# Optimization experiments

Measured on AMD Instinct MI355X. Metric: run time of the kernel, lower is better.

## Reference

```python
import jax, jax.numpy as jnp
import numpy as np


def gru_step(x, h, W, U, b):
    # Keras GRU, reset_after=True. W:[in,3H] U:[H,3H] b:[2,3H]
    gi = x @ W + b[0]
    gh = h @ U + b[1]
    iz, ir, ih = jnp.split(gi, 3, axis=-1)
    hz, hr, hh = jnp.split(gh, 3, axis=-1)
    z = jax.nn.sigmoid(iz + hz)
    r = jax.nn.sigmoid(ir + hr)
    n = jnp.tanh(ih + r * hh)
    return z * h + (1.0 - z) * n


def gru_seq(x, W, U, b):
    # x: [B,S,in] -> outputs [B,S,H], last state [B,H]; zero initial state
    B = x.shape[0]
    H = U.shape[0]
    h0 = jnp.zeros((B, H), x.dtype)
    def step(h, xt):
        h2 = gru_step(xt, h, W, U, b)
        return h2, h2
    hT, ys = jax.lax.scan(step, h0, jnp.swapaxes(x, 0, 1))
    return jnp.swapaxes(ys, 0, 1), hT


def setup_inputs() -> dict:
    key = jax.random.key(0)
    ks = jax.random.split(key, 24)
    V_en, V_fr, E, H = 32000, 32000, 256, 1024
    B, S = 32, 48
    s = 0.05
    d = {}
    d["inputs"] = jax.random.randint(ks[0], (B, S), 0, V_en, dtype=jnp.int32)
    d["gen_seq_len"] = 32
    d["start_id"] = 1
    d["emb_en"] = jax.random.normal(ks[1], (V_en, E), jnp.float32) * s
    d["emb_fr"] = jax.random.normal(ks[2], (V_fr, E), jnp.float32) * s
    # encoder GRUs: layer0 in=E, layer1 in=H
    d["enc_W0"] = jax.random.normal(ks[3], (E, 3 * H), jnp.float32) * s
    d["enc_U0"] = jax.random.normal(ks[4], (H, 3 * H), jnp.float32) * s
    d["enc_b0"] = jnp.zeros((2, 3 * H), jnp.float32)
    d["enc_W1"] = jax.random.normal(ks[5], (H, 3 * H), jnp.float32) * s
    d["enc_U1"] = jax.random.normal(ks[6], (H, 3 * H), jnp.float32) * s
    d["enc_b1"] = jnp.zeros((2, 3 * H), jnp.float32)
    # decoder GRUs: layer0 in = H(context)+E(embed), layer1 in = H
    d["dec_W0"] = jax.random.normal(ks[7], (H + E, 3 * H), jnp.float32) * s
    d["dec_U0"] = jax.random.normal(ks[8], (H, 3 * H), jnp.float32) * s
    d["dec_b0"] = jnp.zeros((2, 3 * H), jnp.float32)
    d["dec_W1"] = jax.random.normal(ks[9], (H, 3 * H), jnp.float32) * s
    d["dec_U1"] = jax.random.normal(ks[10], (H, 3 * H), jnp.float32) * s
    d["dec_b1"] = jnp.zeros((2, 3 * H), jnp.float32)
    # Bahdanau attention
    d["attn_W1"] = jax.random.normal(ks[11], (H, H), jnp.float32) * s
    d["attn_b1"] = jnp.zeros((H,), jnp.float32)
    d["attn_W2"] = jax.random.normal(ks[12], (H, H), jnp.float32) * s
    d["attn_b2"] = jnp.zeros((H,), jnp.float32)
    d["attn_V"] = jax.random.normal(ks[13], (H, 1), jnp.float32) * s
    d["attn_Vb"] = jnp.zeros((1,), jnp.float32)
    # output projection
    d["fc_W"] = jax.random.normal(ks[14], (H, V_fr), jnp.float32) * s
    d["fc_b"] = jnp.zeros((V_fr,), jnp.float32)
    return d


def reference(inputs, gen_seq_len, start_id, emb_en, emb_fr,
              enc_W0, enc_U0, enc_b0, enc_W1, enc_U1, enc_b1,
              dec_W0, dec_U0, dec_b0, dec_W1, dec_U1, dec_b1,
              attn_W1, attn_b1, attn_W2, attn_b2, attn_V, attn_Vb,
              fc_W, fc_b):
    B = inputs.shape[0]
    H = enc_U0.shape[0]
    V_fr = fc_W.shape[1]
    # ---- encoder ----
    x = emb_en[inputs]                       # [B,S,E]
    x, _ = gru_seq(x, enc_W0, enc_U0, enc_b0)
    enc_out, enc_hidden = gru_seq(x, enc_W1, enc_U1, enc_b1)  # [B,S,H], [B,H]
    # precompute W2(values) (same math as recomputing per step)
    enc_proj = enc_out @ attn_W2 + attn_b2   # [B,S,H]
    zeros_h = jnp.zeros((B, H), jnp.float32)

    def dec_step(carry, _):
        dec_in, hidden = carry
        # Bahdanau attention
        q = hidden @ attn_W1 + attn_b1                          # [B,H]
        score = jnp.tanh(q[:, None, :] + enc_proj) @ attn_V + attn_Vb  # [B,S,1]
        w = jax.nn.softmax(score, axis=1)
        ctx = jnp.sum(w * enc_out, axis=1)                      # [B,H]
        xt = jnp.concatenate([ctx, emb_fr[dec_in]], axis=-1)    # [B,H+E]
        # decoder GRUs with state reset to zero each step (initial_state=None)
        h1 = gru_step(xt, zeros_h, dec_W0, dec_U0, dec_b0)
        h2 = gru_step(h1, zeros_h, dec_W1, dec_U1, dec_b1)
        logits = h2 @ fc_W + fc_b                               # [B,V_fr]
        nxt = jnp.argmax(logits, axis=1).astype(jnp.int32)
        return (nxt, h2), logits

    dec_in0 = jnp.full((B,), start_id, dtype=jnp.int32)
    (_, _), logits_seq = jax.lax.scan(dec_step, (dec_in0, enc_hidden),
                                      None, length=gen_seq_len - 1)
    first = jax.nn.one_hot(dec_in0, V_fr, dtype=jnp.float32)[:, None, :]
    return jnp.concatenate([first, jnp.swapaxes(logits_seq, 0, 1)], axis=1)
```

## Files before the change

kernel.cpp:

```cpp
#include <hip/hip_runtime.h>
#include <math.h>

#define BB 32
#define SS 48
#define HH 1024
#define EE 256
#define VOC 32000
#define GEN 32
#define G3 3072
#define CH 256
#define NLOG (VOC / 128)

typedef float v4f __attribute__((ext_vector_type(4)));

__device__ __forceinline__ float sigf(float x) { return 1.f / (1.f + expf(-x)); }

__global__ __launch_bounds__(256) void embed_en_k(const int* __restrict__ inputs,
                                                  const float* __restrict__ emb,
                                                  float* __restrict__ x) {
    int i = blockIdx.x * 256 + threadIdx.x;
    int row = i >> 8;
    int e = i & 255;
    x[i] = emb[(size_t)inputs[row] * EE + e];
}

__global__ __launch_bounds__(256) void transpose_k(const float* __restrict__ U,
                                                   float* __restrict__ UT,
                                                   int R, int C) {
    __shared__ float t[32][33];
    int tx = threadIdx.x & 31, ty = threadIdx.x >> 5;
    int bx = blockIdx.x * 32;
    int by = blockIdx.y * 32;
#pragma unroll
    for (int i = 0; i < 4; ++i)
        t[ty + 8 * i][tx] = U[(size_t)(by + ty + 8 * i) * C + bx + tx];
    __syncthreads();
#pragma unroll
    for (int i = 0; i < 4; ++i)
        UT[(size_t)(bx + ty + 8 * i) * R + by + tx] = t[tx][ty + 8 * i];
}

__global__ __launch_bounds__(256) void gemm64(const float* __restrict__ A,
                                              const float* __restrict__ Bm,
                                              const float* __restrict__ bias,
                                              float* __restrict__ C,
                                              int N, int K) {
    __shared__ float As[32][68];
    __shared__ float Bs[32][68];
    int tid = threadIdx.x;
    int tx = tid & 15, ty = tid >> 4;
    int arow = blockIdx.y * 64, bcol = blockIdx.x * 64;
    int am = tid >> 2;
    int aq = tid & 3;
    int bk = tid >> 4;
    int bn = tid & 15;
    float acc[4][4] = {};
    for (int k0 = 0; k0 < K; k0 += 32) {
        float4 a0 = *(const float4*)(A + (size_t)(arow + am) * K + k0 + aq * 8);
        float4 a1 = *(const float4*)(A + (size_t)(arow + am) * K + k0 + aq * 8 + 4);
        float4 b0 = *(const float4*)(Bm + (size_t)(k0 + bk) * N + bcol + bn * 4);
        float4 b1 = *(const float4*)(Bm + (size_t)(k0 + bk + 16) * N + bcol + bn * 4);
        __syncthreads();
        As[aq * 8 + 0][am] = a0.x; As[aq * 8 + 1][am] = a0.y;
        As[aq * 8 + 2][am] = a0.z; As[aq * 8 + 3][am] = a0.w;
        As[aq * 8 + 4][am] = a1.x; As[aq * 8 + 5][am] = a1.y;
        As[aq * 8 + 6][am] = a1.z; As[aq * 8 + 7][am] = a1.w;
        *(float4*)&Bs[bk][bn * 4] = b0;
        *(float4*)&Bs[bk + 16][bn * 4] = b1;
        __syncthreads();
#pragma unroll
        for (int kk = 0; kk < 32; ++kk) {
            float4 a = *(const float4*)&As[kk][ty * 4];
            float4 b = *(const float4*)&Bs[kk][tx * 4];
            acc[0][0] += a.x * b.x; acc[0][1] += a.x * b.y;
            acc[0][2] += a.x * b.z; acc[0][3] += a.x * b.w;
            acc[1][0] += a.y * b.x; acc[1][1] += a.y * b.y;
            acc[1][2] += a.y * b.z; acc[1][3] += a.y * b.w;
            acc[2][0] += a.z * b.x; acc[2][1] += a.z * b.y;
            acc[2][2] += a.z * b.z; acc[2][3] += a.z * b.w;
            acc[3][0] += a.w * b.x; acc[3][1] += a.w * b.y;
            acc[3][2] += a.w * b.z; acc[3][3] += a.w * b.w;
        }
    }
    float4 bb = *(const float4*)&bias[bcol + tx * 4];
#pragma unroll
    for (int i = 0; i < 4; ++i) {
        size_t row = arow + ty * 4 + i;
        *(float4*)(C + row * N + bcol + tx * 4) =
            make_float4(acc[i][0] + bb.x, acc[i][1] + bb.y,
                        acc[i][2] + bb.z, acc[i][3] + bb.w);
    }
}

__global__ __launch_bounds__(384) void enc_step(
    const float* __restrict__ gi,
    const float* __restrict__ UT,
    const float* __restrict__ b1,
    const float* __restrict__ hin,
    float* __restrict__ hout,
    float* __restrict__ seqout,
    int t) {
    __shared__ float hs[32][260];
    __shared__ float ghs[12][33];
    const int tid = threadIdx.x;
    const int c0 = blockIdx.x * 4;
    const int ks = tid & 31;
    const int outIdx = tid >> 5;
    const int cq = outIdx >> 2;
    const int mo = outIdx & 3;
    const float* Ubase = UT + (size_t)(cq * HH + c0) * HH;
    float acc[4][8];
#pragma unroll
    for (int a = 0; a < 4; ++a)
#pragma unroll
        for (int b = 0; b < 8; ++b) acc[a][b] = 0.f;
    for (int ch = 0; ch < HH / CH; ++ch) {
        for (int i = tid; i < 32 * 64; i += 384) {
            int m = i >> 6, q = i & 63;
            *(float4*)&hs[m][q * 4] =
                *(const float4*)&hin[m * HH + ch * CH + q * 4];
        }
        __syncthreads();
#pragma unroll
        for (int j = 0; j < 2; ++j) {
            int kq = (j * 32 + ks) * 4;
            float4 uv[4];
#pragma unroll
            for (int ci = 0; ci < 4; ++ci)
                uv[ci] = *(const float4*)&Ubase[(size_t)ci * HH + ch * CH + kq];
#pragma unroll
            for (int mi = 0; mi < 8; ++mi) {
                float4 hv = *(const float4*)&hs[mo * 8 + mi][kq];
#pragma unroll
                for (int ci = 0; ci < 4; ++ci)
                    acc[ci][mi] += hv.x * uv[ci].x + hv.y * uv[ci].y +
                                   hv.z * uv[ci].z + hv.w * uv[ci].w;
            }
        }
        __syncthreads();
    }
#pragma unroll
    for (int ci = 0; ci < 4; ++ci)
#pragma unroll
        for (int mi = 0; mi < 8; ++mi) {
            float v = acc[ci][mi];
            v += __shfl_xor(v, 1, 64);
            v += __shfl_xor(v, 2, 64);
            v += __shfl_xor(v, 4, 64);
            v += __shfl_xor(v, 8, 64);
            v += __shfl_xor(v, 16, 64);
            if (ks == 0) ghs[cq * 4 + ci][mo * 8 + mi] = v;
        }
    __syncthreads();
    if (tid < 128) {
        int m = tid & 31, c = tid >> 5;
        int col = c0 + c;
        float ghz = ghs[c][m] + b1[col];
        float ghr = ghs[4 + c][m] + b1[HH + col];
        float ghh = ghs[8 + c][m] + b1[2 * HH + col];
        const float* gir = gi + ((size_t)m * SS + t) * G3;
        float z = sigf(gir[col] + ghz);
        float r = sigf(gir[HH + col] + ghr);
        float nn = tanhf(gir[2 * HH + col] + r * ghh);
        float h = z * hin[m * HH + col] + (1.f - z) * nn;
        hout[m * HH + col] = h;
        seqout[((size_t)m * SS + t) * HH + col] = h;
    }
}

__global__ __launch_bounds__(384) void dec_step(
    const float* __restrict__ xt, int K,
    const float* __restrict__ WT,
    const float* __restrict__ b0, const float* __restrict__ b1,
    float* __restrict__ hout) {
    __shared__ float hs[32][260];
    __shared__ float ghs[12][33];
    const int tid = threadIdx.x;
    const int c0 = blockIdx.x * 4;
    const int ks = tid & 31;
    const int outIdx = tid >> 5;
    const int cq = outIdx >> 2;
    const int mo = outIdx & 3;
    const float* Ubase = WT + (size_t)(cq * HH + c0) * K;
    float acc[4][8];
#pragma unroll
    for (int a = 0; a < 4; ++a)
#pragma unroll
        for (int b = 0; b < 8; ++b) acc[a][b] = 0.f;
    const int nch = K / CH;
    for (int ch = 0; ch < nch; ++ch) {
        for (int i = tid; i < 32 * 64; i += 384) {
            int m = i >> 6, q = i & 63;
            *(float4*)&hs[m][q * 4] =
                *(const float4*)&xt[(size_t)m * K + ch * CH + q * 4];
        }
        __syncthreads();
#pragma unroll
        for (int j = 0; j < 2; ++j) {
            int kq = (j * 32 + ks) * 4;
            float4 uv[4];
#pragma unroll
            for (int ci = 0; ci < 4; ++ci)
                uv[ci] = *(const float4*)&Ubase[(size_t)ci * K + ch * CH + kq];
#pragma unroll
            for (int mi = 0; mi < 8; ++mi) {
                float4 hv = *(const float4*)&hs[mo * 8 + mi][kq];
#pragma unroll
                for (int ci = 0; ci < 4; ++ci)
                    acc[ci][mi] += hv.x * uv[ci].x + hv.y * uv[ci].y +
                                   hv.z * uv[ci].z + hv.w * uv[ci].w;
            }
        }
        __syncthreads();
    }
#pragma unroll
    for (int ci = 0; ci < 4; ++ci)
#pragma unroll
        for (int mi = 0; mi < 8; ++mi) {
            float v = acc[ci][mi];
            v += __shfl_xor(v, 1, 64);
            v += __shfl_xor(v, 2, 64);
            v += __shfl_xor(v, 4, 64);
            v += __shfl_xor(v, 8, 64);
            v += __shfl_xor(v, 16, 64);
            if (ks == 0) ghs[cq * 4 + ci][mo * 8 + mi] = v;
        }
    __syncthreads();
    if (tid < 128) {
        int m = tid & 31, c = tid >> 5;
        int col = c0 + c;
        float z = sigf(ghs[c][m] + b0[col] + b1[col]);
        float r = sigf(ghs[4 + c][m] + b0[HH + col] + b1[HH + col]);
        float nn = tanhf(ghs[8 + c][m] + b0[2 * HH + col] + r * b1[2 * HH + col]);
        hout[m * HH + col] = (1.f - z) * nn;
    }
}

__global__ __launch_bounds__(256) void logits_q(const float* __restrict__ A,
                                                const float* __restrict__ fcW,
                                                const float* __restrict__ fcb,
                                                float* __restrict__ Cl,
                                                const float* __restrict__ qW,
                                                const float* __restrict__ qb,
                                                float* __restrict__ Cq,
                                                float* __restrict__ pmv,
                                                int* __restrict__ pmi,
                                                int qonly) {
    __shared__ float As[32][36];
    __shared__ float Bs[32][132];
    int tid = threadIdx.x;
    int bid = blockIdx.x;
    bool isq = qonly || (bid >= NLOG);
    const float* Bm = isq ? qW : fcW;
    const float* bias = isq ? qb : fcb;
    float* C = isq ? Cq : Cl;
    int N = isq ? HH : VOC;
    int ldc = isq ? HH : GEN * VOC;
    int bcol = (isq ? (qonly ? bid : bid - NLOG) : bid) * 128;
    int nc = tid & 15, mg = (tid >> 4) & 7, ksl = tid >> 7;
    const int nch = HH / 32;
    int am = tid >> 3, aq = tid & 7;
    float4 ra = *(const float4*)(A + (size_t)am * HH + aq * 4);
    float4 rb[4];
#pragma unroll
    for (int it = 0; it < 4; ++it) {
        int lin = it * 256 + tid;
        int k = lin >> 5, q = lin & 31;
        const float* p = Bm + (size_t)k * N + bcol + q * 4;
        if (isq) { rb[it] = *(const float4*)p; }
        else { v4f v = __builtin_nontemporal_load((const v4f*)p); rb[it] = *(float4*)&v; }
    }
    float acc[4][8] = {};
    for (int ch = 0; ch < nch; ++ch) {
        __syncthreads();
        As[aq * 4 + 0][am] = ra.x; As[aq * 4 + 1][am] = ra.y;
        As[aq * 4 + 2][am] = ra.z; As[aq * 4 + 3][am] = ra.w;
#pragma unroll
        for (int it = 0; it < 4; ++it) {
            int lin = it * 256 + tid;
            int k = lin >> 5, q = lin & 31;
            *(float4*)&Bs[k][q * 4] = rb[it];
        }
        __syncthreads();
        if (ch + 1 < nch) {
            int k0 = (ch + 1) * 32;
            ra = *(const float4*)(A + (size_t)am * HH + k0 + aq * 4);
#pragma unroll
            for (int it = 0; it < 4; ++it) {
                int lin = it * 256 + tid;
                int k = lin >> 5, q = lin & 31;
                const float* p = Bm + (size_t)(k0 + k) * N + bcol + q * 4;
                if (isq) { rb[it] = *(const float4*)p; }
                else { v4f v = __builtin_nontemporal_load((const v4f*)p); rb[it] = *(float4*)&v; }
            }
        }
#pragma unroll
        for (int kk = 0; kk < 16; ++kk) {
            int k2 = kk * 2 + ksl;
            float a[4], b[8];
            *(float4*)&a[0] = *(const float4*)&As[k2][mg * 4];
            *(float4*)&b[0] = *(const float4*)&Bs[k2][nc * 8];
            *(float4*)&b[4] = *(const float4*)&Bs[k2][nc * 8 + 4];
#pragma unroll
            for (int r = 0; r < 4; ++r)
#pragma unroll
                for (int j = 0; j < 8; ++j) acc[r][j] += a[r] * b[j];
        }
    }
    __syncthreads();
    float* red = &Bs[0][0];
    if (ksl == 1) {
        int p = tid & 127;
#pragma unroll
        for (int r = 0; r < 4; ++r)
#pragma unroll
            for (int j = 0; j < 8; ++j) red[p * 32 + r * 8 + j] = acc[r][j];
    }
    __syncthreads();
    if (ksl == 0) {
        int p = tid;
#pragma unroll
        for (int r = 0; r < 4; ++r)
#pragma unroll
            for (int j = 0; j < 8; ++j) acc[r][j] += red[p * 32 + r * 8 + j];
        float bb[8];
        *(float4*)&bb[0] = *(const float4*)&bias[bcol + nc * 8];
        *(float4*)&bb[4] = *(const float4*)&bias[bcol + nc * 8 + 4];
#pragma unroll
        for (int r = 0; r < 4; ++r) {
#pragma unroll
            for (int j = 0; j < 8; ++j) acc[r][j] += bb[j];
            int row = mg * 4 + r;
            float* cp = C + (size_t)row * ldc + bcol + nc * 8;
            if (isq) {
                *(float4*)cp = make_float4(acc[r][0], acc[r][1], acc[r][2], acc[r][3]);
                *(float4*)(cp + 4) = make_float4(acc[r][4], acc[r][5], acc[r][6], acc[r][7]);
            } else {
                v4f o0 = {acc[r][0], acc[r][1], acc[r][2], acc[r][3]};
                v4f o1 = {acc[r][4], acc[r][5], acc[r][6], acc[r][7]};
                __builtin_nontemporal_store(o0, (v4f*)cp);
                __builtin_nontemporal_store(o1, (v4f*)(cp + 4));
            }
        }
        if (!isq) {
#pragma unroll
            for (int r = 0; r < 4; ++r) {
                float best = acc[r][0]; int bidx = bcol + nc * 8;
#pragma unroll
                for (int j = 1; j < 8; ++j)
                    if (acc[r][j] > best) { best = acc[r][j]; bidx = bcol + nc * 8 + j; }
#pragma unroll
                for (int o = 1; o < 16; o <<= 1) {
                    float pv = __shfl_xor(best, o, 64);
                    int pi = __shfl_xor(bidx, o, 64);
                    if (pv > best || (pv == best && pi < bidx)) { best = pv; bidx = pi; }
                }
                if (nc == 0) {
                    int row = mg * 4 + r;
                    pmv[row * NLOG + bid] = best;
                    pmi[row * NLOG + bid] = bidx;
                }
            }
        }
    }
}

__global__ __launch_bounds__(512) void attn_ctx(const float* __restrict__ qb,
                                                const float* __restrict__ enc_proj,
                                                const float* __restrict__ enc_out,
                                                const float* __restrict__ vvec,
                                                const float* __restrict__ vb,
                                                const float* __restrict__ emb_fr,
                                                const int* __restrict__ start_id,
                                                const float* __restrict__ pmv,
                                                const int* __restrict__ pmi,
                                                int nb,
                                                float* __restrict__ xt) {
    int b = blockIdx.x;
    int tid = threadIdx.x;
    int wave = tid >> 6, lane = tid & 63;
    __shared__ float sc[SS];
    __shared__ float wsm[SS];
    __shared__ float sv[256];
    __shared__ int si[256];
    __shared__ int stok;
    if (nb == 0) {
        if (tid == 0) stok = start_id[0];
    } else {
        if (tid < 256) {
            float best = -3.4e38f; int bi = 0x7fffffff;
            for (int i = tid; i < nb; i += 256) {
                float v = pmv[(size_t)b * nb + i];
                int ix = pmi[(size_t)b * nb + i];
                if (v > best || (v == best && ix < bi)) { best = v; bi = ix; }
            }
            sv[tid] = best; si[tid] = bi;
        }
        __syncthreads();
        for (int s = 128; s; s >>= 1) {
            if (tid < s) {
                if (sv[tid + s] > sv[tid] ||
                    (sv[tid + s] == sv[tid] && si[tid + s] < si[tid])) {
                    sv[tid] = sv[tid + s]; si[tid] = si[tid + s];
                }
            }
            __syncthreads();
        }
        if (tid == 0) stok = si[0];
    }
    const float* q = qb + (size_t)b * HH;
    for (int s = wave; s < SS; s += 8) {
        const float* ep = enc_proj + (size_t)(b * SS + s) * HH;
        float sum = 0.f;
        for (int h = lane; h < HH; h += 64)
            sum += tanhf(q[h] + ep[h]) * vvec[h];
#pragma unroll
        for (int o = 32; o; o >>= 1) sum += __shfl_xor(sum, o, 64);
        if (lane == 0) sc[s] = sum + vb[0];
    }
    __syncthreads();
    if (tid < 64) {
        float v = (lane < SS) ? sc[lane] : -3.4e38f;
        float m = v;
#pragma unroll
        for (int o = 32; o; o >>= 1) m = fmaxf(m, __shfl_xor(m, o, 64));
        float e = (lane < SS) ? expf(v - m) : 0.f;
        float ssum = e;
#pragma unroll
        for (int o = 32; o; o >>= 1) ssum += __shfl_xor(ssum, o, 64);
        if (lane < SS) wsm[lane] = e / ssum;
    }
    __syncthreads();
    if (tid < 256) {
        float4 cx = make_float4(0.f, 0.f, 0.f, 0.f);
#pragma unroll 4
        for (int s = 0; s < SS; ++s) {
            float w = wsm[s];
            float4 e = *(const float4*)&enc_out[(size_t)(b * SS + s) * HH + tid * 4];
            cx.x += w * e.x; cx.y += w * e.y; cx.z += w * e.z; cx.w += w * e.w;
        }
        *(float4*)&xt[(size_t)b * (HH + EE) + tid * 4] = cx;
        xt[(size_t)b * (HH + EE) + HH + tid] = emb_fr[(size_t)stok * EE + tid];
    }
}

__global__ __launch_bounds__(256) void init_dec(float* __restrict__ out,
                                                const int* __restrict__ start_id) {
    int idx = blockIdx.x * 256 + threadIdx.x;
    int sid = start_id[0];
    int b = idx / VOC, v = idx % VOC;
    out[(size_t)b * (GEN * VOC) + v] = (v == sid) ? 1.f : 0.f;
}

extern "C" void kernel_launch(void* const* d_in, const int* in_sizes, int n_in,
                              void* d_out, int out_size, void* d_ws, size_t ws_size,
                              hipStream_t stream) {
    const int*   inputs   = (const int*)d_in[0];
    const int*   start_id = (const int*)d_in[2];
    const float* emb_en   = (const float*)d_in[3];
    const float* emb_fr   = (const float*)d_in[4];
    const float* enc_W0   = (const float*)d_in[5];
    const float* enc_U0   = (const float*)d_in[6];
    const float* enc_b0   = (const float*)d_in[7];
    const float* enc_W1   = (const float*)d_in[8];
    const float* enc_U1   = (const float*)d_in[9];
    const float* enc_b1   = (const float*)d_in[10];
    const float* dec_W0   = (const float*)d_in[11];
    const float* dec_b0   = (const float*)d_in[13];
    const float* dec_W1   = (const float*)d_in[14];
    const float* dec_b1   = (const float*)d_in[16];
    const float* attn_W1  = (const float*)d_in[17];
    const float* attn_b1  = (const float*)d_in[18];
    const float* attn_W2  = (const float*)d_in[19];
    const float* attn_b2  = (const float*)d_in[20];
    const float* attn_V   = (const float*)d_in[21];
    const float* attn_Vb  = (const float*)d_in[22];
    const float* fc_W     = (const float*)d_in[23];
    const float* fc_b     = (const float*)d_in[24];
    float* out = (float*)d_out;
    float* ws  = (float*)d_ws;

    float* giA   = ws;
    float* x_emb = giA + (size_t)BB * SS * G3;
    float* seq0  = x_emb + (size_t)BB * SS * EE;
    float* encO  = seq0 + (size_t)BB * SS * HH;
    float* encP  = encO + (size_t)BB * SS * HH;
    float* h0A   = encP + (size_t)BB * SS * HH;
    float* h0B   = h0A + BB * HH;
    float* h1A   = h0B + BB * HH;
    float* h1B   = h1A + BB * HH;
    float* qbuf  = h1B + BB * HH;
    float* xt    = qbuf + BB * HH;
    float* h1buf = xt + BB * (HH + EE);
    float* pmv   = h1buf + BB * HH;
    int*   pmi   = (int*)(pmv + 32 * NLOG);
    float* U0T   = (float*)(pmi + 32 * NLOG);
    float* U1T   = U0T + (size_t)G3 * HH;
    float* W0Td  = giA;
    float* W1Td  = U0T;

    embed_en_k<<<(BB * SS * EE) / 256, 256, 0, stream>>>(inputs, emb_en, x_emb);
    gemm64<<<dim3(G3 / 64, (BB * SS) / 64), 256, 0, stream>>>(
        x_emb, enc_W0, enc_b0, giA, G3, EE);
    transpose_k<<<dim3(96, 32), 256, 0, stream>>>(enc_U0, U0T, HH, G3);
    transpose_k<<<dim3(96, 32), 256, 0, stream>>>(enc_U1, U1T, HH, G3);
    hipMemsetAsync(h0A, 0, BB * HH * sizeof(float), stream);
    for (int t = 0; t < SS; ++t) {
        const float* hin = (t & 1) ? h0B : h0A;
        float* hout = (t & 1) ? h0A : h0B;
        enc_step<<<256, 384, 0, stream>>>(giA, U0T, enc_b0 + G3, hin, hout, seq0, t);
    }
    gemm64<<<dim3(G3 / 64, (BB * SS) / 64), 256, 0, stream>>>(
        seq0, enc_W1, enc_b1, giA, G3, HH);
    hipMemsetAsync(h1A, 0, BB * HH * sizeof(float), stream);
    for (int t = 0; t < SS; ++t) {
        const float* hin = (t & 1) ? h1B : h1A;
        float* hout = (t & 1) ? h1A : h1B;
        enc_step<<<256, 384, 0, stream>>>(giA, U1T, enc_b1 + G3, hin, hout, encO, t);
    }
    gemm64<<<dim3(HH / 64, (BB * SS) / 64), 256, 0, stream>>>(
        encO, attn_W2, attn_b2, encP, HH, HH);

    transpose_k<<<dim3(96, 40), 256, 0, stream>>>(dec_W0, W0Td, HH + EE, G3);
    transpose_k<<<dim3(96, 32), 256, 0, stream>>>(dec_W1, W1Td, HH, G3);

    init_dec<<<(BB * VOC) / 256, 256, 0, stream>>>(out, start_id);
    logits_q<<<HH / 128, 256, 0, stream>>>(h1A, fc_W, fc_b, out,
                                           attn_W1, attn_b1, qbuf, pmv, pmi, 1);
    for (int step = 1; step < GEN; ++step) {
        attn_ctx<<<BB, 512, 0, stream>>>(qbuf, encP, encO, attn_V, attn_Vb,
                                         emb_fr, start_id, pmv, pmi,
                                         (step == 1) ? 0 : NLOG, xt);
        dec_step<<<256, 384, 0, stream>>>(xt, HH + EE, W0Td, dec_b0,
                                          dec_b0 + G3, h1buf);
        dec_step<<<256, 384, 0, stream>>>(h1buf, HH, W1Td, dec_b1,
                                          dec_b1 + G3, h1A);
        logits_q<<<NLOG + HH / 128, 256, 0, stream>>>(h1A, fc_W, fc_b,
                                                      out + (size_t)step * VOC,
                                                      attn_W1, attn_b1, qbuf,
                                                      pmv, pmi, 0);
    }
}
```

Before: 7.155 ms.

## Precompute encoder outputs times decoder W0 and fuse attention into decoder layer0

Uses linearity: ctx@W0[:H] equals the attention weights times (enc_out@W0[:H]), so a one-time GEMM precomputes P = encO @ dec_W0 for every source position. Each decode step then needs only a 48-term weighted sum over P plus the embedding part, in place of a 1280x3072 matvec per batch row. Attention scoring, softmax, argmax token selection and the layer-0 GRU gates are fused into one kernel, which removes the attn_ctx launch and the xt round trip. The cost is extra recomputation, since the score and softmax for each batch row are now redone by all 8 column blocks. It also changes summation order.

```diff
diff --git a/kernel.cpp b/kernel.cpp
--- a/kernel.cpp
+++ b/kernel.cpp
@@ -233,6 +233,97 @@
         float r = sigf(ghs[4 + c][m] + b0[HH + col] + b1[HH + col]);
         float nn = tanhf(ghs[8 + c][m] + b0[2 * HH + col] + r * b1[2 * HH + col]);
         hout[m * HH + col] = (1.f - z) * nn;
+    }
+}
+
+__global__ __launch_bounds__(384) void dec_front(
+    const float* __restrict__ qb, const float* __restrict__ encP,
+    const float* __restrict__ vvec, const float* __restrict__ vb,
+    const float* __restrict__ emb_fr, const int* __restrict__ start_id,
+    const float* __restrict__ pmv, const int* __restrict__ pmi, int nb,
+    const float* __restrict__ P, const float* __restrict__ W0,
+    const float* __restrict__ b0, const float* __restrict__ b1,
+    float* __restrict__ h1out) {
+    __shared__ float sc[SS];
+    __shared__ float wsm[SS];
+    __shared__ float sv[256];
+    __shared__ int si[256];
+    __shared__ int stok;
+    __shared__ float embl[EE];
+    __shared__ float g[3][128];
+    const int tid = threadIdx.x;
+    const int b = blockIdx.x & 31;
+    const int j0 = (blockIdx.x >> 5) * 128;
+    const int wave = tid >> 6, lane = tid & 63;
+    if (nb == 0) {
+        if (tid == 0) stok = start_id[0];
+    } else {
+        if (tid < 256) {
+            float best = -3.4e38f; int bi = 0x7fffffff;
+            for (int i = tid; i < nb; i += 256) {
+                float v = pmv[(size_t)b * nb + i];
+                int ix = pmi[(size_t)b * nb + i];
+                if (v > best || (v == best && ix < bi)) { best = v; bi = ix; }
+            }
+            sv[tid] = best; si[tid] = bi;
+        }
+        __syncthreads();
+        for (int s = 128; s; s >>= 1) {
+            if (tid < s) {
+                if (sv[tid + s] > sv[tid] ||
+                    (sv[tid + s] == sv[tid] && si[tid + s] < si[tid])) {
+                    sv[tid] = sv[tid + s]; si[tid] = si[tid + s];
+                }
+            }
+            __syncthreads();
+        }
+        if (tid == 0) stok = si[0];
+    }
+    __syncthreads();
+    if (tid < EE) embl[tid] = emb_fr[(size_t)stok * EE + tid];
+    const float* q = qb + (size_t)b * HH;
+    for (int s = wave; s < SS; s += 6) {
+        const float* ep = encP + (size_t)(b * SS + s) * HH;
+        float sum = 0.f;
+        for (int h = lane; h < HH; h += 64)
+            sum += tanhf(q[h] + ep[h]) * vvec[h];
+#pragma unroll
+        for (int o = 32; o; o >>= 1) sum += __shfl_xor(sum, o, 64);
+        if (lane == 0) sc[s] = sum + vb[0];
+    }
+    __syncthreads();
+    if (tid < 64) {
+        float v = (lane < SS) ? sc[lane] : -3.4e38f;
+        float m = v;
+#pragma unroll
+        for (int o = 32; o; o >>= 1) m = fmaxf(m, __shfl_xor(m, o, 64));
+        float e = (lane < SS) ? expf(v - m) : 0.f;
+        float ssum = e;
+#pragma unroll
+        for (int o = 32; o; o >>= 1) ssum += __shfl_xor(ssum, o, 64);
+        if (lane < SS) wsm[lane] = e / ssum;
+    }
+    __syncthreads();
+    {
+        int gate = tid >> 7;
+        int col = tid & 127;
+        int gcol = gate * HH + j0 + col;
+        float acc = b0[gcol];
+        const float* Pb = P + (size_t)b * SS * G3 + gcol;
+#pragma unroll 8
+        for (int s = 0; s < SS; ++s) acc += wsm[s] * Pb[(size_t)s * G3];
+        const float* Wb = W0 + (size_t)HH * G3 + gcol;
+#pragma unroll 8
+        for (int k = 0; k < EE; ++k) acc += embl[k] * Wb[(size_t)k * G3];
+        g[gate][col] = acc;
+    }
+    __syncthreads();
+    if (tid < 128) {
+        int jj = j0 + tid;
+        float z = sigf(g[0][tid] + b1[jj]);
+        float r = sigf(g[1][tid] + b1[HH + jj]);
+        float nn = tanhf(g[2][tid] + r * b1[2 * HH + jj]);
+        h1out[(size_t)b * HH + jj] = (1.f - z) * nn;
     }
 }
 
@@ -362,85 +453,6 @@
                 }
             }
         }
-    }
-}
-
-__global__ __launch_bounds__(512) void attn_ctx(const float* __restrict__ qb,
-                                                const float* __restrict__ enc_proj,
-                                                const float* __restrict__ enc_out,
-                                                const float* __restrict__ vvec,
-                                                const float* __restrict__ vb,
-                                                const float* __restrict__ emb_fr,
-                                                const int* __restrict__ start_id,
-                                                const float* __restrict__ pmv,
-                                                const int* __restrict__ pmi,
-                                                int nb,
-                                                float* __restrict__ xt) {
-    int b = blockIdx.x;
-    int tid = threadIdx.x;
-    int wave = tid >> 6, lane = tid & 63;
-    __shared__ float sc[SS];
-    __shared__ float wsm[SS];
-    __shared__ float sv[256];
-    __shared__ int si[256];
-    __shared__ int stok;
-    if (nb == 0) {
-        if (tid == 0) stok = start_id[0];
-    } else {
-        if (tid < 256) {
-            float best = -3.4e38f; int bi = 0x7fffffff;
-            for (int i = tid; i < nb; i += 256) {
-                float v = pmv[(size_t)b * nb + i];
-                int ix = pmi[(size_t)b * nb + i];
-                if (v > best || (v == best && ix < bi)) { best = v; bi = ix; }
-            }
-            sv[tid] = best; si[tid] = bi;
-        }
-        __syncthreads();
-        for (int s = 128; s; s >>= 1) {
-            if (tid < s) {
-                if (sv[tid + s] > sv[tid] ||
-                    (sv[tid + s] == sv[tid] && si[tid + s] < si[tid])) {
-                    sv[tid] = sv[tid + s]; si[tid] = si[tid + s];
-                }
-            }
-            __syncthreads();
-        }
-        if (tid == 0) stok = si[0];
-    }
-    const float* q = qb + (size_t)b * HH;
-    for (int s = wave; s < SS; s += 8) {
-        const float* ep = enc_proj + (size_t)(b * SS + s) * HH;
-        float sum = 0.f;
-        for (int h = lane; h < HH; h += 64)
-            sum += tanhf(q[h] + ep[h]) * vvec[h];
-#pragma unroll
-        for (int o = 32; o; o >>= 1) sum += __shfl_xor(sum, o, 64);
-        if (lane == 0) sc[s] = sum + vb[0];
-    }
-    __syncthreads();
-    if (tid < 64) {
-        float v = (lane < SS) ? sc[lane] : -3.4e38f;
-        float m = v;
-#pragma unroll
-        for (int o = 32; o; o >>= 1) m = fmaxf(m, __shfl_xor(m, o, 64));
-        float e = (lane < SS) ? expf(v - m) : 0.f;
-        float ssum = e;
-#pragma unroll
-        for (int o = 32; o; o >>= 1) ssum += __shfl_xor(ssum, o, 64);
-        if (lane < SS) wsm[lane] = e / ssum;
-    }
-    __syncthreads();
-    if (tid < 256) {
-        float4 cx = make_float4(0.f, 0.f, 0.f, 0.f);
-#pragma unroll 4
-        for (int s = 0; s < SS; ++s) {
-            float w = wsm[s];
-            float4 e = *(const float4*)&enc_out[(size_t)(b * SS + s) * HH + tid * 4];
-            cx.x += w * e.x; cx.y += w * e.y; cx.z += w * e.z; cx.w += w * e.w;
-        }
-        *(float4*)&xt[(size_t)b * (HH + EE) + tid * 4] = cx;
-        xt[(size_t)b * (HH + EE) + HH + tid] = emb_fr[(size_t)stok * EE + tid];
     }
 }
 
@@ -490,14 +502,14 @@
     float* h1A   = h0B + BB * HH;
     float* h1B   = h1A + BB * HH;
     float* qbuf  = h1B + BB * HH;
-    float* xt    = qbuf + BB * HH;
-    float* h1buf = xt + BB * (HH + EE);
+    float* h1buf = qbuf + BB * HH;
     float* pmv   = h1buf + BB * HH;
     int*   pmi   = (int*)(pmv + 32 * NLOG);
     float* U0T   = (float*)(pmi + 32 * NLOG);
     float* U1T   = U0T + (size_t)G3 * HH;
-    float* W0Td  = giA;
+    float* Pmat  = giA;
     float* W1Td  = U0T;
+    float* zb    = h1B;
 
     embed_en_k<<<(BB * SS * EE) / 256, 256, 0, stream>>>(inputs, emb_en, x_emb);
     gemm64<<<dim3(G3 / 64, (BB * SS) / 64), 256, 0, stream>>>(
@@ -521,18 +533,20 @@
     gemm64<<<dim3(HH / 64, (BB * SS) / 64), 256, 0, stream>>>(
         encO, attn_W2, attn_b2, encP, HH, HH);
 
-    transpose_k<<<dim3(96, 40), 256, 0, stream>>>(dec_W0, W0Td, HH + EE, G3);
     transpose_k<<<dim3(96, 32), 256, 0, stream>>>(dec_W1, W1Td, HH, G3);
+    hipMemsetAsync(zb, 0, G3 * sizeof(float), stream);
+    gemm64<<<dim3(G3 / 64, (BB * SS) / 64), 256, 0, stream>>>(
+        encO, dec_W0, zb, Pmat, G3, HH);
 
     init_dec<<<(BB * VOC) / 256, 256, 0, stream>>>(out, start_id);
     logits_q<<<HH / 128, 256, 0, stream>>>(h1A, fc_W, fc_b, out,
                                            attn_W1, attn_b1, qbuf, pmv, pmi, 1);
     for (int step = 1; step < GEN; ++step) {
-        attn_ctx<<<BB, 512, 0, stream>>>(qbuf, encP, encO, attn_V, attn_Vb,
-                                         emb_fr, start_id, pmv, pmi,
-                                         (step == 1) ? 0 : NLOG, xt);
-        dec_step<<<256, 384, 0, stream>>>(xt, HH + EE, W0Td, dec_b0,
-                                          dec_b0 + G3, h1buf);
+        dec_front<<<256, 384, 0, stream>>>(qbuf, encP, attn_V, attn_Vb,
+                                           emb_fr, start_id, pmv, pmi,
+                                           (step == 1) ? 0 : NLOG,
+                                           Pmat, dec_W0, dec_b0, dec_b0 + G3,
+                                           h1buf);
         dec_step<<<256, 384, 0, stream>>>(h1buf, HH, W1Td, dec_b1,
                                           dec_b1 + G3, h1A);
         logits_q<<<NLOG + HH / 128, 256, 0, stream>>>(h1A, fc_W, fc_b,
```

Measured after the change: 6.995 ms (median of 2 runs). -2.2%, faster.
